# Kernel tuning notes

Measured on AMD Instinct MI355X. Metric: run time of the kernel, lower is better.

## Reference

```python
import jax, jax.numpy as jnp
import numpy as np

N = 20000   # nodes
E = 160000  # edges
D = 128     # out_dim == in_dim
H = 8       # heads
DK = D // H # 16


def setup_inputs() -> dict:
    key = jax.random.key(0)
    ks = jax.random.split(key, 16)
    f = lambda i, shape, s=1.0: jax.random.normal(ks[i], shape, dtype=jnp.float32) * s
    z = lambda shape: jnp.zeros(shape, dtype=jnp.float32)
    return {
        "x_txt": f(0, (N, D)), "x_img": f(1, (N, D)), "x_s": f(2, (N, D)),
        "Wk": f(3, (D, D), 0.05), "bk": z((D,)),
        "Wq": f(4, (D, D), 0.05), "bq": z((D,)),
        "Wv": f(5, (D, D), 0.05), "bv": z((D,)),
        "Wa": f(6, (D, D), 0.05), "ba": z((D,)),
        "rel_att": f(7, (H, DK, DK), 0.25),
        "rel_msg": f(8, (H, DK, DK), 0.25),
        "rel_pri": jnp.ones((H,), jnp.float32),
        "wm_txt": f(9, (H, DK, DK), 0.25),
        "wm_img": f(10, (H, DK, DK), 0.25),
        "wm_s": f(11, (H, DK, DK), 0.25),
        "skip": jnp.ones((1,), jnp.float32),
        "src": jax.random.randint(ks[12], (E,), 0, N),
        "dst": jax.random.randint(ks[13], (E,), 0, N),
    }


def reference(x_txt, x_img, x_s, Wk, bk, Wq, bq, Wv, bv, Wa, ba,
              rel_att, rel_msg, rel_pri, wm_txt, wm_img, wm_s, skip, src, dst):
    n_heads, dk = rel_att.shape[0], rel_att.shape[1]
    n_nodes = x_txt.shape[0]
    sqrt_dk = jnp.sqrt(jnp.asarray(dk, jnp.float32))

    def proj(x, W, b):
        return (x @ W + b).reshape(n_nodes, n_heads, dk)

    xs = (x_txt, x_img, x_s)
    k = [proj(x, Wk, bk)[src] for x in xs]  # [E,H,dk] gathered at src
    q = [proj(x, Wq, bq)[dst] for x in xs]  # [E,H,dk] gathered at dst
    v = [proj(x, Wv, bv)[src] for x in xs]

    # cross-modal lambda: per-edge modality alignment softmax (over the 3 modalities)
    wm = (wm_txt, wm_img, wm_s)
    lam_scores = jnp.stack(
        [jnp.einsum('ehd,hdf,ehf->eh', k[m], wm[m], q[m]) for m in range(3)], axis=0)
    lam = jax.nn.softmax(lam_scores, axis=0)  # [3,E,H]

    # edge attention logits (scaled *10 as in reduce_func) and relation-msg values
    att = [jnp.einsum('ehd,hdf,ehf->eh', k[m], rel_att, q[m]) * rel_pri / sqrt_dk * 10.0
           for m in range(3)]
    vmsg = [jnp.einsum('ehd,hdf->ehf', v[m], rel_msg) for m in range(3)]

    align = -(jnp.abs(att[0] - att[1]) + jnp.abs(att[0] - att[2])
              + jnp.abs(att[1] - att[2])) / 3.0

    def seg_softmax(x):  # softmax over edges sharing the same dst node
        m = jax.ops.segment_max(x, dst, num_segments=n_nodes)
        m = jnp.where(jnp.isfinite(m), m, 0.0)
        e = jnp.exp(x - m[dst])
        s = jax.ops.segment_sum(e, dst, num_segments=n_nodes)
        s = jnp.where(s == 0.0, 1.0, s)
        return e / s[dst]

    beta2 = seg_softmax(align)
    sm = [seg_softmax(a) for a in att]
    beta1 = sm[0] * lam[0] + sm[1] * lam[1] + sm[2] * lam[2]
    beta = seg_softmax(beta1 * beta2)  # [E,H]

    alpha = jax.nn.sigmoid(skip)  # [1]
    outs = []
    for m in range(3):
        h = jax.ops.segment_sum(beta[..., None] * vmsg[m], dst,
                                num_segments=n_nodes).reshape(n_nodes, -1)
        outs.append((h @ Wa + ba) * alpha + xs[m] * (1.0 - alpha))
    return tuple(outs)
```

## Files before the change

### kernel.cpp

```cpp
#include <hip/hip_runtime.h>

#define D 128
#define NH 8

typedef __bf16 bf16x8 __attribute__((ext_vector_type(8)));
typedef unsigned short ushortx8 __attribute__((ext_vector_type(8)));
typedef float floatx4 __attribute__((ext_vector_type(4)));

__device__ __forceinline__ float bf2f(unsigned short u) {
  union { unsigned int i; float f; } x; x.i = ((unsigned int)u) << 16; return x.f;
}
__device__ __forceinline__ unsigned short f2bf(float f) {
  union { float f; unsigned int i; } x; x.f = f;
  unsigned int i = x.i;
  return (unsigned short)((i + 0x7FFFu + ((i >> 16) & 1u)) >> 16);
}
__device__ __forceinline__ void acc2(unsigned int ku, unsigned int qu, float& s) {
  union { unsigned int i; float f; } a, b;
  a.i = ku << 16;          b.i = qu << 16;          s += a.f * b.f;
  a.i = ku & 0xffff0000u;  b.i = qu & 0xffff0000u;  s += a.f * b.f;
}

__global__ __launch_bounds__(256) void k_misc(
    const float* __restrict__ Wk, const float* __restrict__ bk,
    const float* __restrict__ Wq, const float* __restrict__ bq,
    const float* __restrict__ Wv, const float* __restrict__ bv,
    const float* __restrict__ rel_att, const float* __restrict__ rel_msg,
    const float* __restrict__ rel_pri,
    const float* __restrict__ wm0, const float* __restrict__ wm1,
    const float* __restrict__ wm2,
    unsigned short* __restrict__ Wt_all, float* __restrict__ bias_all,
    const int* __restrict__ dst, int* __restrict__ counts, int E)
{
  int b = blockIdx.x;
  if (b >= 384) {
    int e = (b - 384) * 256 + threadIdx.x;
    if (e < E) atomicAdd(&counts[dst[e]], 1);
    return;
  }
  int gid = b * 256 + threadIdx.x;
  if (gid >= 6 * 128 * 128) return;
  int p = gid >> 14;
  int idx = gid & 16383;
  int c = idx >> 7, k = idx & 127;
  int h = c >> 4, r = c & 15;
  float wsum = 0.f, bsum = 0.f;
  if (p == 0) {
    wsum = Wk[k * 128 + c];
    bsum = bk[c];
  } else if (p <= 4) {
    const float* M = (p == 1) ? rel_att : ((p == 2) ? wm0 : ((p == 3) ? wm1 : wm2));
#pragma unroll
    for (int f = 0; f < 16; f++) {
      float mv = M[h * 256 + r * 16 + f];
      wsum += Wq[k * 128 + h * 16 + f] * mv;
      bsum += bq[h * 16 + f] * mv;
    }
    if (p == 1) { float sc = rel_pri[h] * 2.5f; wsum *= sc; bsum *= sc; }
  } else {
#pragma unroll
    for (int d = 0; d < 16; d++) {
      float mv = rel_msg[h * 256 + d * 16 + r];
      wsum += Wv[k * 128 + h * 16 + d] * mv;
      bsum += bv[h * 16 + d] * mv;
    }
  }
  Wt_all[(size_t)p * 16384 + c * 128 + k] = f2bf(wsum);
  if (k == 0) bias_all[p * 128 + c] = bsum;
}

__global__ __launch_bounds__(512) void k_proj(
    const float* __restrict__ x0, const float* __restrict__ x1,
    const float* __restrict__ x2,
    const unsigned short* __restrict__ Wt_all, const float* __restrict__ bias_all,
    unsigned short* __restrict__ P,
    const int* __restrict__ counts, int* __restrict__ row_start,
    int* __restrict__ alloc, int N)
{
  if (blockIdx.y == 3) {
    if (blockIdx.x != 0) return;
    int tid = threadIdx.x, lane = tid & 63;
    for (int base = 0; base < N; base += 512) {
      int n = base + tid;
      int cnt = (n < N) ? counts[n] : 0;
      int x = cnt;
#pragma unroll
      for (int off = 1; off < 64; off <<= 1) {
        int y = __shfl_up(x, off, 64);
        if (lane >= off) x += y;
      }
      int wtot = __shfl(x, 63, 64);
      int wbase = 0;
      if (lane == 63) wbase = atomicAdd(alloc, wtot);
      wbase = __shfl(wbase, 63, 64);
      if (n < N) row_start[n] = wbase + x - cnt;
    }
    return;
  }
  __shared__ __attribute__((aligned(16))) unsigned short Wt[128 * 136];
  int m = blockIdx.y;
  const float* X = (m == 0) ? x0 : ((m == 1) ? x1 : x2);
  int tid = threadIdx.x;
  int wave = tid >> 6, lane = tid & 63;
  int quad = lane >> 4, l16 = lane & 15;
  int row0 = blockIdx.x * 128 + wave * 16;
  int arow = row0 + l16; if (arow >= N) arow = N - 1;
  const float* ap = X + (size_t)arow * D;
  bf16x8 afr[4];
#pragma unroll
  for (int kk4 = 0; kk4 < 4; kk4++) {
    float4 f0 = *(const float4*)(ap + kk4 * 32 + quad * 8);
    float4 f1 = *(const float4*)(ap + kk4 * 32 + quad * 8 + 4);
    ushortx8 uu;
    uu[0]=f2bf(f0.x); uu[1]=f2bf(f0.y); uu[2]=f2bf(f0.z); uu[3]=f2bf(f0.w);
    uu[4]=f2bf(f1.x); uu[5]=f2bf(f1.y); uu[6]=f2bf(f1.z); uu[7]=f2bf(f1.w);
    afr[kk4] = __builtin_bit_cast(bf16x8, uu);
  }
  for (int pt = 0; pt < 4; pt++) {
    int wp = (pt == 0) ? 0 : ((pt == 1) ? 1 : ((pt == 2) ? (2 + m) : 5));
    const unsigned short* Wsrc = Wt_all + (size_t)wp * 16384;
    const float* B = bias_all + wp * 128;
    __syncthreads();
#pragma unroll
    for (int it = 0; it < 4; it++) {
      int idx = it * 512 + tid;
      int c = idx >> 4, kc = (idx & 15) << 3;
      *(uint4*)(&Wt[c * 136 + kc]) = *(const uint4*)(&Wsrc[c * 128 + kc]);
    }
    __syncthreads();
    floatx4 acc[8];
#pragma unroll
    for (int ct = 0; ct < 8; ct++) acc[ct] = (floatx4)0.f;
#pragma unroll
    for (int kk4 = 0; kk4 < 4; kk4++) {
#pragma unroll
      for (int ct = 0; ct < 8; ct++) {
        uint4 bu = *(const uint4*)(&Wt[(ct * 16 + l16) * 136 + kk4 * 32 + quad * 8]);
        bf16x8 bf = __builtin_bit_cast(bf16x8, bu);
        acc[ct] = __builtin_amdgcn_mfma_f32_16x16x32_bf16(afr[kk4], bf, acc[ct], 0, 0, 0);
      }
    }
    unsigned short* Pout = P + (size_t)(pt * 3 + m) * N * D;
#pragma unroll
    for (int ct = 0; ct < 8; ct++) {
      int col = ct * 16 + l16;
      float bias = B[col];
#pragma unroll
      for (int i = 0; i < 4; i++) {
        int r = row0 + quad * 4 + i;
        if (r < N) Pout[(size_t)r * D + col] = f2bf(acc[ct][i] + bias);
      }
    }
  }
}

__global__ void k_scatter(const int* __restrict__ dst, const int* __restrict__ src,
                          const int* __restrict__ row_start,
                          int* __restrict__ cursor, int* __restrict__ src_sorted, int E) {
  int e = blockIdx.x * 256 + threadIdx.x;
  if (e < E) {
    int d = dst[e];
    int pos = atomicAdd(&cursor[d], 1);
    src_sorted[row_start[d] + pos] = src[e];
  }
}

__device__ __forceinline__ void edge_vals(
    const unsigned short* __restrict__ P, size_t Nsz, int s, int h,
    const uint4 (&qa)[3][2], const uint4 (&qw)[3][2],
    float (&av)[3], float (&lv)[3])
{
#pragma unroll
  for (int m = 0; m < 3; m++) {
    const unsigned short* kp = P + ((size_t)m * Nsz + s) * 128 + h * 16;
    uint4 k0 = *(const uint4*)kp, k1 = *(const uint4*)(kp + 8);
    const unsigned int* ka = (const unsigned int*)&k0;
    const unsigned int* kb = (const unsigned int*)&k1;
    const unsigned int* a0 = (const unsigned int*)&qa[m][0];
    const unsigned int* a1 = (const unsigned int*)&qa[m][1];
    const unsigned int* w0 = (const unsigned int*)&qw[m][0];
    const unsigned int* w1 = (const unsigned int*)&qw[m][1];
    float da = 0.f, dw = 0.f;
#pragma unroll
    for (int j = 0; j < 4; j++) {
      acc2(ka[j], a0[j], da); acc2(kb[j], a1[j], da);
      acc2(ka[j], w0[j], dw); acc2(kb[j], w1[j], dw);
    }
    av[m] = da;
    lv[m] = dw;
  }
  float mx = fmaxf(lv[0], fmaxf(lv[1], lv[2]));
  float e0 = __expf(lv[0] - mx), e1 = __expf(lv[1] - mx), e2 = __expf(lv[2] - mx);
  float inv = 1.f / (e0 + e1 + e2);
  lv[0] = e0 * inv; lv[1] = e1 * inv; lv[2] = e2 * inv;
}

__global__ __launch_bounds__(256) void k_node(
    const unsigned short* __restrict__ P,
    const int* __restrict__ row_start, const int* __restrict__ counts,
    const int* __restrict__ srcs,
    unsigned short* __restrict__ hagg, int N, int E)
{
  int tid = threadIdx.x;
  int wave = tid >> 6, lane = tid & 63;
  int n = blockIdx.x * 4 + wave;
  if (n >= N) return;
  int ro = row_start[n];
  int deg = counts[n];
  float acc00 = 0, acc01 = 0, acc10 = 0, acc11 = 0, acc20 = 0, acc21 = 0;
  if (deg > 0) {
    int h = lane & 7, slot = lane >> 3;
    size_t Nsz = (size_t)N;
    uint4 qa[3][2], qw[3][2];
#pragma unroll
    for (int m = 0; m < 3; m++) {
      const unsigned short* qap = P + ((size_t)(3 + m) * Nsz + n) * 128 + h * 16;
      const unsigned short* qwp = P + ((size_t)(6 + m) * Nsz + n) * 128 + h * 16;
      qa[m][0] = *(const uint4*)qap; qa[m][1] = *(const uint4*)(qap + 8);
      qw[m][0] = *(const uint4*)qwp; qw[m][1] = *(const uint4*)(qwp + 8);
    }
    int nch = (deg + 7) >> 3;
    float cX0[4] = {}, cX1[4] = {}, cX2[4] = {}, cEa[4] = {}, cT[4] = {};
    int cS[4] = {};
    float sA0 = 0, sA1 = 0, sA2 = 0, sAl = 0;
#pragma unroll
    for (int c = 0; c < 4; c++) {
      int idx = c * 8 + slot;
      if (c < nch && idx < deg) {
        int s = srcs[ro + idx]; cS[c] = s;
        float av[3], lv[3];
        edge_vals(P, Nsz, s, h, qa, qw, av, lv);
        float e0 = __expf(av[0]), e1 = __expf(av[1]), e2 = __expf(av[2]);
        float align = -(fabsf(av[0]-av[1]) + fabsf(av[0]-av[2]) + fabsf(av[1]-av[2])) * (1.f/3.f);
        float ea = __expf(align);
        cX0[c] = lv[0] * e0; cX1[c] = lv[1] * e1; cX2[c] = lv[2] * e2; cEa[c] = ea;
        sA0 += e0; sA1 += e1; sA2 += e2; sAl += ea;
      }
    }
    for (int c = 4; c < nch; c++) {
      int idx = c * 8 + slot;
      if (idx < deg) {
        int s = srcs[ro + idx];
        float av[3], lv[3];
        edge_vals(P, Nsz, s, h, qa, qw, av, lv);
        float align = -(fabsf(av[0]-av[1]) + fabsf(av[0]-av[2]) + fabsf(av[1]-av[2])) * (1.f/3.f);
        sA0 += __expf(av[0]); sA1 += __expf(av[1]); sA2 += __expf(av[2]);
        sAl += __expf(align);
      }
    }
#pragma unroll
    for (int off = 8; off < 64; off <<= 1) {
      sA0 += __shfl_xor(sA0, off, 64);
      sA1 += __shfl_xor(sA1, off, 64);
      sA2 += __shfl_xor(sA2, off, 64);
      sAl += __shfl_xor(sAl, off, 64);
    }
    float rA0 = 1.f / fmaxf(sA0, 1e-30f), rA1 = 1.f / fmaxf(sA1, 1e-30f);
    float rA2 = 1.f / fmaxf(sA2, 1e-30f), rAl = 1.f / fmaxf(sAl, 1e-30f);
    float sT = 0;
#pragma unroll
    for (int c = 0; c < 4; c++) {
      int idx = c * 8 + slot;
      if (c < nch && idx < deg) {
        float t = (cX0[c] * rA0 + cX1[c] * rA1 + cX2[c] * rA2) * (cEa[c] * rAl);
        cT[c] = t;
        sT += __expf(t);
      }
    }
    for (int c = 4; c < nch; c++) {
      int idx = c * 8 + slot;
      if (idx < deg) {
        int s = srcs[ro + idx];
        float av[3], lv[3];
        edge_vals(P, Nsz, s, h, qa, qw, av, lv);
        float align = -(fabsf(av[0]-av[1]) + fabsf(av[0]-av[2]) + fabsf(av[1]-av[2])) * (1.f/3.f);
        float t = (lv[0]*__expf(av[0])*rA0 + lv[1]*__expf(av[1])*rA1 + lv[2]*__expf(av[2])*rA2)
                  * (__expf(align) * rAl);
        sT += __expf(t);
      }
    }
#pragma unroll
    for (int off = 8; off < 64; off <<= 1) sT += __shfl_xor(sT, off, 64);
    float rT = 1.f / fmaxf(sT, 1e-30f);
    const unsigned int* Pu = (const unsigned int*)P;
    int hl = lane >> 3;
#pragma unroll
    for (int c = 0; c < 4; c++) {
      if (c < nch) {
        int idx = c * 8 + slot;
        float beta = (idx < deg) ? __expf(cT[c]) * rT : 0.f;
        int sv = cS[c];
        float bj[8]; int sj[8];
#pragma unroll
        for (int jj = 0; jj < 8; jj++) {
          bj[jj] = __shfl(beta, jj * 8 + hl, 64);
          sj[jj] = __shfl(sv, jj * 8, 64);
        }
#pragma unroll
        for (int jj = 0; jj < 8; jj++) {
          size_t base9 = ((size_t)9 * Nsz + sj[jj]) * 64 + lane;
          unsigned int u0 = Pu[base9];
          unsigned int u1 = Pu[base9 + Nsz * 64];
          unsigned int u2 = Pu[base9 + 2 * Nsz * 64];
          float b = bj[jj];
          acc00 += b * bf2f((unsigned short)u0); acc01 += b * bf2f((unsigned short)(u0 >> 16));
          acc10 += b * bf2f((unsigned short)u1); acc11 += b * bf2f((unsigned short)(u1 >> 16));
          acc20 += b * bf2f((unsigned short)u2); acc21 += b * bf2f((unsigned short)(u2 >> 16));
        }
      }
    }
    for (int c = 4; c < nch; c++) {
      int idx = c * 8 + slot;
      float beta = 0.f; int sv = 0;
      if (idx < deg) {
        sv = srcs[ro + idx];
        float av[3], lv[3];
        edge_vals(P, Nsz, sv, h, qa, qw, av, lv);
        float align = -(fabsf(av[0]-av[1]) + fabsf(av[0]-av[2]) + fabsf(av[1]-av[2])) * (1.f/3.f);
        float t = (lv[0]*__expf(av[0])*rA0 + lv[1]*__expf(av[1])*rA1 + lv[2]*__expf(av[2])*rA2)
                  * (__expf(align) * rAl);
        beta = __expf(t) * rT;
      }
      int jmax = min(8, deg - c * 8);
      for (int jj = 0; jj < jmax; jj++) {
        float b = __shfl(beta, jj * 8 + hl, 64);
        int s = __shfl(sv, jj * 8, 64);
        size_t base9 = ((size_t)9 * Nsz + s) * 64 + lane;
        unsigned int u0 = Pu[base9];
        unsigned int u1 = Pu[base9 + Nsz * 64];
        unsigned int u2 = Pu[base9 + 2 * Nsz * 64];
        acc00 += b * bf2f((unsigned short)u0); acc01 += b * bf2f((unsigned short)(u0 >> 16));
        acc10 += b * bf2f((unsigned short)u1); acc11 += b * bf2f((unsigned short)(u1 >> 16));
        acc20 += b * bf2f((unsigned short)u2); acc21 += b * bf2f((unsigned short)(u2 >> 16));
      }
    }
  }
  unsigned int* ho = (unsigned int*)hagg;
  ho[((size_t)0 * N + n) * 64 + lane] = ((unsigned int)f2bf(acc01) << 16) | f2bf(acc00);
  ho[((size_t)1 * N + n) * 64 + lane] = ((unsigned int)f2bf(acc11) << 16) | f2bf(acc10);
  ho[((size_t)2 * N + n) * 64 + lane] = ((unsigned int)f2bf(acc21) << 16) | f2bf(acc20);
}

__global__ __launch_bounds__(512) void k_out(
    const unsigned short* __restrict__ Hagg, const float* __restrict__ Wa,
    const float* __restrict__ ba,
    const float* __restrict__ x0, const float* __restrict__ x1,
    const float* __restrict__ x2, const float* __restrict__ skip,
    float* __restrict__ out, int N)
{
  __shared__ __attribute__((aligned(16))) unsigned short Wt[128 * 136];
  int m = blockIdx.y;
  const float* X = (m == 0) ? x0 : ((m == 1) ? x1 : x2);
  int tid = threadIdx.x;
#pragma unroll
  for (int it = 0; it < 8; it++) {
    int idx = it * 512 + tid;
    int k = idx >> 5, c4 = (idx & 31) << 2;
    float4 w = *(const float4*)(&Wa[k * 128 + c4]);
    Wt[(c4 + 0) * 136 + k] = f2bf(w.x);
    Wt[(c4 + 1) * 136 + k] = f2bf(w.y);
    Wt[(c4 + 2) * 136 + k] = f2bf(w.z);
    Wt[(c4 + 3) * 136 + k] = f2bf(w.w);
  }
  __syncthreads();
  float alpha = 1.f / (1.f + __expf(-skip[0]));
  float oma = 1.f - alpha;
  int wave = tid >> 6, lane = tid & 63;
  int quad = lane >> 4, l16 = lane & 15;
  int row0 = blockIdx.x * 128 + wave * 16;
  int arow = row0 + l16; if (arow >= N) arow = N - 1;
  const unsigned short* hp = Hagg + ((size_t)m * N + arow) * D;
  floatx4 acc[8];
#pragma unroll
  for (int ct = 0; ct < 8; ct++) acc[ct] = (floatx4)0.f;
#pragma unroll
  for (int kk = 0; kk < 128; kk += 32) {
    uint4 au = *(const uint4*)(hp + kk + quad * 8);
    bf16x8 af = __builtin_bit_cast(bf16x8, au);
#pragma unroll
    for (int ct = 0; ct < 8; ct++) {
      uint4 bu = *(const uint4*)(&Wt[(ct * 16 + l16) * 136 + kk + quad * 8]);
      bf16x8 bf = __builtin_bit_cast(bf16x8, bu);
      acc[ct] = __builtin_amdgcn_mfma_f32_16x16x32_bf16(af, bf, acc[ct], 0, 0, 0);
    }
  }
  float* om = out + (size_t)m * N * D;
#pragma unroll
  for (int ct = 0; ct < 8; ct++) {
    int col = ct * 16 + l16;
    float bias = ba[col];
#pragma unroll
    for (int i = 0; i < 4; i++) {
      int r = row0 + quad * 4 + i;
      if (r < N) {
        om[(size_t)r * D + col] =
            (acc[ct][i] + bias) * alpha + X[(size_t)r * D + col] * oma;
      }
    }
  }
}

extern "C" void kernel_launch(void* const* d_in, const int* in_sizes, int n_in,
                              void* d_out, int out_size, void* d_ws, size_t ws_size,
                              hipStream_t stream) {
  const float* x0 = (const float*)d_in[0];
  const float* x1 = (const float*)d_in[1];
  const float* x2 = (const float*)d_in[2];
  const float* Wk = (const float*)d_in[3];
  const float* bk = (const float*)d_in[4];
  const float* Wq = (const float*)d_in[5];
  const float* bq = (const float*)d_in[6];
  const float* Wv = (const float*)d_in[7];
  const float* bv = (const float*)d_in[8];
  const float* Wa = (const float*)d_in[9];
  const float* ba = (const float*)d_in[10];
  const float* rel_att = (const float*)d_in[11];
  const float* rel_msg = (const float*)d_in[12];
  const float* rel_pri = (const float*)d_in[13];
  const float* wm0 = (const float*)d_in[14];
  const float* wm1 = (const float*)d_in[15];
  const float* wm2 = (const float*)d_in[16];
  const float* skip = (const float*)d_in[17];
  const int* src = (const int*)d_in[18];
  const int* dstv = (const int*)d_in[19];
  int N = in_sizes[0] / D;
  int E = in_sizes[18];

  char* wsb = (char*)d_ws;
  size_t off = 0;
  auto alloc_b = [&](size_t bytes) { size_t o = off; off += (bytes + 63) & ~(size_t)63; return o; };
  unsigned short* P         = (unsigned short*)(wsb + alloc_b((size_t)12 * N * D * 2));
  unsigned short* Wt_all    = (unsigned short*)(wsb + alloc_b((size_t)6 * 16384 * 2));
  float*          bias_all  = (float*)(wsb + alloc_b((size_t)6 * 128 * 4));
  int*            cnt2      = (int*)(wsb + alloc_b(((size_t)2 * N + 64) * 4));
  int*            row_start = (int*)(wsb + alloc_b((size_t)(N + 1) * 4));
  int*            src_sorted= (int*)(wsb + alloc_b((size_t)E * 4));
  unsigned short* hagg      = (unsigned short*)(wsb + alloc_b((size_t)3 * N * D * 2));
  int* counts = cnt2;
  int* cursor = cnt2 + N;
  int* allocc = cnt2 + 2 * N;

  hipMemsetAsync(cnt2, 0, ((size_t)2 * N + 64) * sizeof(int), stream);
  int hist_blocks = (E + 255) / 256;
  k_misc<<<dim3(384 + hist_blocks), 256, 0, stream>>>(
      Wk, bk, Wq, bq, Wv, bv, rel_att, rel_msg, rel_pri, wm0, wm1, wm2,
      Wt_all, bias_all, dstv, counts, E);
  k_proj<<<dim3((N + 127) / 128, 4), 512, 0, stream>>>(
      x0, x1, x2, Wt_all, bias_all, P, counts, row_start, allocc, N);
  k_scatter<<<dim3((E + 255) / 256), 256, 0, stream>>>(
      dstv, src, row_start, cursor, src_sorted, E);
  k_node<<<dim3((N + 3) / 4), 256, 0, stream>>>(
      P, row_start, counts, src_sorted, hagg, N, E);
  k_out<<<dim3((N + 127) / 128, 3), 512, 0, stream>>>(
      hagg, Wa, ba, x0, x1, x2, skip, (float*)d_out, N);
}
```

Baseline: 255.5 us.

## Fuse all stages into a persistent megakernel with grid-wide barriers

Replaces the five separate launches and their memset with one persistent kernel sized from occupancy, where stages are separated by atomic-counter grid barriers. Projection and output GEMM tiles drop to 64 rows with 256-thread blocks, and the CSR prefix scan is spread across waves in parallel instead of running in a single block. The scatter cursor is initialised to row_start, so the extra add and the memset of the cursor array go away. The aim is to cut launch gaps and the serial scan, at the cost of barrier spin overhead and a dependence on every block being co-resident.

New measurement: 248.8 us. -2.6%, faster.

```diff
diff --git a/kernel.cpp b/kernel.cpp
--- a/kernel.cpp
+++ b/kernel.cpp
@@ -21,7 +21,19 @@
   a.i = ku & 0xffff0000u;  b.i = qu & 0xffff0000u;  s += a.f * b.f;
 }
 
-__global__ __launch_bounds__(256) void k_misc(
+__device__ __forceinline__ void gbar(int* cnt, int nb) {
+  __threadfence();
+  __syncthreads();
+  if (threadIdx.x == 0) {
+    __hip_atomic_fetch_add(cnt, 1, __ATOMIC_ACQ_REL, __HIP_MEMORY_SCOPE_AGENT);
+    while (__hip_atomic_load(cnt, __ATOMIC_ACQUIRE, __HIP_MEMORY_SCOPE_AGENT) < nb) {}
+  }
+  __syncthreads();
+  __threadfence();
+}
+
+__device__ __forceinline__ void fold_item(
+    int gid,
     const float* __restrict__ Wk, const float* __restrict__ bk,
     const float* __restrict__ Wq, const float* __restrict__ bq,
     const float* __restrict__ Wv, const float* __restrict__ bv,
@@ -29,17 +41,8 @@
     const float* __restrict__ rel_pri,
     const float* __restrict__ wm0, const float* __restrict__ wm1,
     const float* __restrict__ wm2,
-    unsigned short* __restrict__ Wt_all, float* __restrict__ bias_all,
-    const int* __restrict__ dst, int* __restrict__ counts, int E)
-{
-  int b = blockIdx.x;
-  if (b >= 384) {
-    int e = (b - 384) * 256 + threadIdx.x;
-    if (e < E) atomicAdd(&counts[dst[e]], 1);
-    return;
-  }
-  int gid = b * 256 + threadIdx.x;
-  if (gid >= 6 * 128 * 128) return;
+    unsigned short* __restrict__ Wt_all, float* __restrict__ bias_all)
+{
   int p = gid >> 14;
   int idx = gid & 16383;
   int c = idx >> 7, k = idx & 127;
@@ -69,41 +72,17 @@
   if (k == 0) bias_all[p * 128 + c] = bsum;
 }
 
-__global__ __launch_bounds__(512) void k_proj(
-    const float* __restrict__ x0, const float* __restrict__ x1,
+__device__ __forceinline__ void proj_tile(
+    int t, const float* __restrict__ x0, const float* __restrict__ x1,
     const float* __restrict__ x2,
     const unsigned short* __restrict__ Wt_all, const float* __restrict__ bias_all,
-    unsigned short* __restrict__ P,
-    const int* __restrict__ counts, int* __restrict__ row_start,
-    int* __restrict__ alloc, int N)
-{
-  if (blockIdx.y == 3) {
-    if (blockIdx.x != 0) return;
-    int tid = threadIdx.x, lane = tid & 63;
-    for (int base = 0; base < N; base += 512) {
-      int n = base + tid;
-      int cnt = (n < N) ? counts[n] : 0;
-      int x = cnt;
-#pragma unroll
-      for (int off = 1; off < 64; off <<= 1) {
-        int y = __shfl_up(x, off, 64);
-        if (lane >= off) x += y;
-      }
-      int wtot = __shfl(x, 63, 64);
-      int wbase = 0;
-      if (lane == 63) wbase = atomicAdd(alloc, wtot);
-      wbase = __shfl(wbase, 63, 64);
-      if (n < N) row_start[n] = wbase + x - cnt;
-    }
-    return;
-  }
-  __shared__ __attribute__((aligned(16))) unsigned short Wt[128 * 136];
-  int m = blockIdx.y;
+    unsigned short* __restrict__ P, int N, unsigned short* Wt, int tid)
+{
+  int m = t % 3, rt = t / 3;
   const float* X = (m == 0) ? x0 : ((m == 1) ? x1 : x2);
-  int tid = threadIdx.x;
   int wave = tid >> 6, lane = tid & 63;
   int quad = lane >> 4, l16 = lane & 15;
-  int row0 = blockIdx.x * 128 + wave * 16;
+  int row0 = rt * 64 + wave * 16;
   int arow = row0 + l16; if (arow >= N) arow = N - 1;
   const float* ap = X + (size_t)arow * D;
   bf16x8 afr[4];
@@ -122,8 +101,8 @@
     const float* B = bias_all + wp * 128;
     __syncthreads();
 #pragma unroll
-    for (int it = 0; it < 4; it++) {
-      int idx = it * 512 + tid;
+    for (int it = 0; it < 8; it++) {
+      int idx = it * 256 + tid;
       int c = idx >> 4, kc = (idx & 15) << 3;
       *(uint4*)(&Wt[c * 136 + kc]) = *(const uint4*)(&Wsrc[c * 128 + kc]);
     }
@@ -154,15 +133,23 @@
   }
 }
 
-__global__ void k_scatter(const int* __restrict__ dst, const int* __restrict__ src,
-                          const int* __restrict__ row_start,
-                          int* __restrict__ cursor, int* __restrict__ src_sorted, int E) {
-  int e = blockIdx.x * 256 + threadIdx.x;
-  if (e < E) {
-    int d = dst[e];
-    int pos = atomicAdd(&cursor[d], 1);
-    src_sorted[row_start[d] + pos] = src[e];
-  }
+__device__ __forceinline__ void assign_chunk(
+    int a, const int* __restrict__ counts, int* __restrict__ row_start,
+    int* __restrict__ cursor, int* __restrict__ allocg, int N, int lane)
+{
+  int n = a * 64 + lane;
+  int cnt = (n < N) ? counts[n] : 0;
+  int x = cnt;
+#pragma unroll
+  for (int off = 1; off < 64; off <<= 1) {
+    int y = __shfl_up(x, off, 64);
+    if (lane >= off) x += y;
+  }
+  int wtot = __shfl(x, 63, 64);
+  int wbase = 0;
+  if (lane == 63) wbase = atomicAdd(allocg, wtot);
+  wbase = __shfl(wbase, 63, 64);
+  if (n < N) { int v = wbase + x - cnt; row_start[n] = v; cursor[n] = v; }
 }
 
 __device__ __forceinline__ void edge_vals(
@@ -195,16 +182,12 @@
   lv[0] = e0 * inv; lv[1] = e1 * inv; lv[2] = e2 * inv;
 }
 
-__global__ __launch_bounds__(256) void k_node(
-    const unsigned short* __restrict__ P,
+__device__ __forceinline__ void node_one(
+    int n, const unsigned short* __restrict__ P,
     const int* __restrict__ row_start, const int* __restrict__ counts,
-    const int* __restrict__ srcs,
-    unsigned short* __restrict__ hagg, int N, int E)
-{
-  int tid = threadIdx.x;
-  int wave = tid >> 6, lane = tid & 63;
-  int n = blockIdx.x * 4 + wave;
-  if (n >= N) return;
+    const int* __restrict__ srcs, unsigned short* __restrict__ hagg,
+    int N, int lane)
+{
   int ro = row_start[n];
   int deg = counts[n];
   float acc00 = 0, acc01 = 0, acc10 = 0, acc11 = 0, acc20 = 0, acc21 = 0;
@@ -341,20 +324,101 @@
   ho[((size_t)2 * N + n) * 64 + lane] = ((unsigned int)f2bf(acc21) << 16) | f2bf(acc20);
 }
 
-__global__ __launch_bounds__(512) void k_out(
-    const unsigned short* __restrict__ Hagg, const float* __restrict__ Wa,
-    const float* __restrict__ ba,
+__device__ __forceinline__ void out_tile(
+    int t, const unsigned short* __restrict__ Hagg, const float* __restrict__ ba,
     const float* __restrict__ x0, const float* __restrict__ x1,
-    const float* __restrict__ x2, const float* __restrict__ skip,
-    float* __restrict__ out, int N)
+    const float* __restrict__ x2, float alpha,
+    float* __restrict__ out, int N, const unsigned short* Wt, int tid)
+{
+  int m = t % 3, rt = t / 3;
+  const float* X = (m == 0) ? x0 : ((m == 1) ? x1 : x2);
+  float oma = 1.f - alpha;
+  int wave = tid >> 6, lane = tid & 63;
+  int quad = lane >> 4, l16 = lane & 15;
+  int row0 = rt * 64 + wave * 16;
+  int arow = row0 + l16; if (arow >= N) arow = N - 1;
+  const unsigned short* hp = Hagg + ((size_t)m * N + arow) * D;
+  floatx4 acc[8];
+#pragma unroll
+  for (int ct = 0; ct < 8; ct++) acc[ct] = (floatx4)0.f;
+#pragma unroll
+  for (int kk = 0; kk < 128; kk += 32) {
+    uint4 au = *(const uint4*)(hp + kk + quad * 8);
+    bf16x8 af = __builtin_bit_cast(bf16x8, au);
+#pragma unroll
+    for (int ct = 0; ct < 8; ct++) {
+      uint4 bu = *(const uint4*)(&Wt[(ct * 16 + l16) * 136 + kk + quad * 8]);
+      bf16x8 bf = __builtin_bit_cast(bf16x8, bu);
+      acc[ct] = __builtin_amdgcn_mfma_f32_16x16x32_bf16(af, bf, acc[ct], 0, 0, 0);
+    }
+  }
+  float* om = out + (size_t)m * N * D;
+#pragma unroll
+  for (int ct = 0; ct < 8; ct++) {
+    int col = ct * 16 + l16;
+    float bias = ba[col];
+#pragma unroll
+    for (int i = 0; i < 4; i++) {
+      int r = row0 + quad * 4 + i;
+      if (r < N) {
+        om[(size_t)r * D + col] =
+            (acc[ct][i] + bias) * alpha + X[(size_t)r * D + col] * oma;
+      }
+    }
+  }
+}
+
+__global__ __launch_bounds__(256) void k_mega(
+    const float* x0, const float* x1, const float* x2,
+    const float* Wk, const float* bk, const float* Wq, const float* bq,
+    const float* Wv, const float* bv, const float* Wa, const float* ba,
+    const float* rel_att, const float* rel_msg, const float* rel_pri,
+    const float* wm0, const float* wm1, const float* wm2,
+    const float* skip, const int* src, const int* dst,
+    float* out, unsigned short* P, unsigned short* Wt_all, float* bias_all,
+    int* bar, int* allocg, int* counts, int* cursor, int* row_start,
+    int* src_sorted, unsigned short* hagg, int N, int E)
 {
   __shared__ __attribute__((aligned(16))) unsigned short Wt[128 * 136];
-  int m = blockIdx.y;
-  const float* X = (m == 0) ? x0 : ((m == 1) ? x1 : x2);
-  int tid = threadIdx.x;
-#pragma unroll
-  for (int it = 0; it < 8; it++) {
-    int idx = it * 512 + tid;
+  int tid = threadIdx.x, bid = blockIdx.x, NB = gridDim.x;
+  int gid = bid * 256 + tid, gstride = NB * 256;
+  int wave = tid >> 6, lane = tid & 63;
+
+  for (int i = gid; i < N; i += gstride) counts[i] = 0;
+  for (int i = gid; i < 6 * 16384; i += gstride)
+    fold_item(i, Wk, bk, Wq, bq, Wv, bv, rel_att, rel_msg, rel_pri,
+              wm0, wm1, wm2, Wt_all, bias_all);
+  gbar(bar + 0 * 16, NB);
+
+  for (int e = gid; e < E; e += gstride) atomicAdd(&counts[dst[e]], 1);
+  int ntiles = ((N + 63) / 64) * 3;
+  for (int t = bid; t < ntiles; t += NB)
+    proj_tile(t, x0, x1, x2, Wt_all, bias_all, P, N, Wt, tid);
+  gbar(bar + 1 * 16, NB);
+
+  int nchunks = (N + 63) / 64;
+  for (int a = bid * 4 + wave; a < nchunks; a += NB * 4)
+    assign_chunk(a, counts, row_start, cursor, allocg, N, lane);
+  gbar(bar + 2 * 16, NB);
+
+  for (int e = gid; e < E; e += gstride) {
+    int d = dst[e];
+    int pos = atomicAdd(&cursor[d], 1);
+    src_sorted[pos] = src[e];
+  }
+  gbar(bar + 3 * 16, NB);
+
+  int ngroups = (N + 3) / 4;
+  for (int g = bid; g < ngroups; g += NB) {
+    int n = g * 4 + wave;
+    if (n < N) node_one(n, P, row_start, counts, src_sorted, hagg, N, lane);
+  }
+  gbar(bar + 4 * 16, NB);
+
+  __syncthreads();
+#pragma unroll
+  for (int it = 0; it < 16; it++) {
+    int idx = it * 256 + tid;
     int k = idx >> 5, c4 = (idx & 31) << 2;
     float4 w = *(const float4*)(&Wa[k * 128 + c4]);
     Wt[(c4 + 0) * 136 + k] = f2bf(w.x);
@@ -364,40 +428,86 @@
   }
   __syncthreads();
   float alpha = 1.f / (1.f + __expf(-skip[0]));
-  float oma = 1.f - alpha;
-  int wave = tid >> 6, lane = tid & 63;
-  int quad = lane >> 4, l16 = lane & 15;
-  int row0 = blockIdx.x * 128 + wave * 16;
-  int arow = row0 + l16; if (arow >= N) arow = N - 1;
-  const unsigned short* hp = Hagg + ((size_t)m * N + arow) * D;
-  floatx4 acc[8];
-#pragma unroll
-  for (int ct = 0; ct < 8; ct++) acc[ct] = (floatx4)0.f;
-#pragma unroll
-  for (int kk = 0; kk < 128; kk += 32) {
-    uint4 au = *(const uint4*)(hp + kk + quad * 8);
-    bf16x8 af = __builtin_bit_cast(bf16x8, au);
-#pragma unroll
-    for (int ct = 0; ct < 8; ct++) {
-      uint4 bu = *(const uint4*)(&Wt[(ct * 16 + l16) * 136 + kk + quad * 8]);
-      bf16x8 bf = __builtin_bit_cast(bf16x8, bu);
-      acc[ct] = __builtin_amdgcn_mfma_f32_16x16x32_bf16(af, bf, acc[ct], 0, 0, 0);
-    }
-  }
-  float* om = out + (size_t)m * N * D;
-#pragma unroll
-  for (int ct = 0; ct < 8; ct++) {
-    int col = ct * 16 + l16;
-    float bias = ba[col];
-#pragma unroll
-    for (int i = 0; i < 4; i++) {
-      int r = row0 + quad * 4 + i;
-      if (r < N) {
-        om[(size_t)r * D + col] =
-            (acc[ct][i] + bias) * alpha + X[(size_t)r * D + col] * oma;
-      }
-    }
-  }
+  for (int t = bid; t < ntiles; t += NB)
+    out_tile(t, hagg, ba, x0, x1, x2, alpha, out, N, Wt, tid);
+}
+
+__global__ __launch_bounds__(256) void fb_misc(
+    const float* Wk, const float* bk, const float* Wq, const float* bq,
+    const float* Wv, const float* bv,
+    const float* rel_att, const float* rel_msg, const float* rel_pri,
+    const float* wm0, const float* wm1, const float* wm2,
+    unsigned short* Wt_all, float* bias_all,
+    const int* dst, int* counts, int E)
+{
+  int b = blockIdx.x;
+  if (b < 384) {
+    int g = b * 256 + threadIdx.x;
+    if (g < 6 * 16384)
+      fold_item(g, Wk, bk, Wq, bq, Wv, bv, rel_att, rel_msg, rel_pri,
+                wm0, wm1, wm2, Wt_all, bias_all);
+  } else {
+    int e = (b - 384) * 256 + threadIdx.x;
+    if (e < E) atomicAdd(&counts[dst[e]], 1);
+  }
+}
+
+__global__ __launch_bounds__(256) void fb_projassign(
+    const float* x0, const float* x1, const float* x2,
+    const unsigned short* Wt_all, const float* bias_all,
+    unsigned short* P, const int* counts, int* row_start, int* cursor,
+    int* allocg, int N)
+{
+  __shared__ __attribute__((aligned(16))) unsigned short Wt[128 * 136];
+  int ntiles = ((N + 63) / 64) * 3;
+  int b = blockIdx.x;
+  if (b < ntiles) {
+    proj_tile(b, x0, x1, x2, Wt_all, bias_all, P, N, Wt, threadIdx.x);
+  } else {
+    int a = (b - ntiles) * 4 + (threadIdx.x >> 6);
+    if (a < (N + 63) / 64)
+      assign_chunk(a, counts, row_start, cursor, allocg, N, threadIdx.x & 63);
+  }
+}
+
+__global__ void fb_scatter(const int* dst, const int* src, int* cursor,
+                           int* src_sorted, int E) {
+  int e = blockIdx.x * 256 + threadIdx.x;
+  if (e < E) {
+    int d = dst[e];
+    int pos = atomicAdd(&cursor[d], 1);
+    src_sorted[pos] = src[e];
+  }
+}
+
+__global__ __launch_bounds__(256) void fb_node(
+    const unsigned short* P, const int* row_start, const int* counts,
+    const int* srcs, unsigned short* hagg, int N)
+{
+  int n = blockIdx.x * 4 + (threadIdx.x >> 6);
+  if (n < N) node_one(n, P, row_start, counts, srcs, hagg, N, threadIdx.x & 63);
+}
+
+__global__ __launch_bounds__(256) void fb_out(
+    const unsigned short* Hagg, const float* Wa, const float* ba,
+    const float* x0, const float* x1, const float* x2, const float* skip,
+    float* out, int N)
+{
+  __shared__ __attribute__((aligned(16))) unsigned short Wt[128 * 136];
+  int tid = threadIdx.x;
+#pragma unroll
+  for (int it = 0; it < 16; it++) {
+    int idx = it * 256 + tid;
+    int k = idx >> 5, c4 = (idx & 31) << 2;
+    float4 w = *(const float4*)(&Wa[k * 128 + c4]);
+    Wt[(c4 + 0) * 136 + k] = f2bf(w.x);
+    Wt[(c4 + 1) * 136 + k] = f2bf(w.y);
+    Wt[(c4 + 2) * 136 + k] = f2bf(w.z);
+    Wt[(c4 + 3) * 136 + k] = f2bf(w.w);
+  }
+  __syncthreads();
+  float alpha = 1.f / (1.f + __expf(-skip[0]));
+  out_tile(blockIdx.x, Hagg, ba, x0, x1, x2, alpha, out, N, Wt, tid);
 }
 
 extern "C" void kernel_launch(void* const* d_in, const int* in_sizes, int n_in,
@@ -432,25 +542,40 @@
   unsigned short* P         = (unsigned short*)(wsb + alloc_b((size_t)12 * N * D * 2));
   unsigned short* Wt_all    = (unsigned short*)(wsb + alloc_b((size_t)6 * 16384 * 2));
   float*          bias_all  = (float*)(wsb + alloc_b((size_t)6 * 128 * 4));
-  int*            cnt2      = (int*)(wsb + alloc_b(((size_t)2 * N + 64) * 4));
+  int*            ctrl      = (int*)(wsb + alloc_b(((size_t)144 + 2 * N) * 4));
   int*            row_start = (int*)(wsb + alloc_b((size_t)(N + 1) * 4));
   int*            src_sorted= (int*)(wsb + alloc_b((size_t)E * 4));
   unsigned short* hagg      = (unsigned short*)(wsb + alloc_b((size_t)3 * N * D * 2));
-  int* counts = cnt2;
-  int* cursor = cnt2 + N;
-  int* allocc = cnt2 + 2 * N;
-
-  hipMemsetAsync(cnt2, 0, ((size_t)2 * N + 64) * sizeof(int), stream);
-  int hist_blocks = (E + 255) / 256;
-  k_misc<<<dim3(384 + hist_blocks), 256, 0, stream>>>(
-      Wk, bk, Wq, bq, Wv, bv, rel_att, rel_msg, rel_pri, wm0, wm1, wm2,
-      Wt_all, bias_all, dstv, counts, E);
-  k_proj<<<dim3((N + 127) / 128, 4), 512, 0, stream>>>(
-      x0, x1, x2, Wt_all, bias_all, P, counts, row_start, allocc, N);
-  k_scatter<<<dim3((E + 255) / 256), 256, 0, stream>>>(
-      dstv, src, row_start, cursor, src_sorted, E);
-  k_node<<<dim3((N + 3) / 4), 256, 0, stream>>>(
-      P, row_start, counts, src_sorted, hagg, N, E);
-  k_out<<<dim3((N + 127) / 128, 3), 512, 0, stream>>>(
-      hagg, Wa, ba, x0, x1, x2, skip, (float*)d_out, N);
-}
+  int* bar    = ctrl;
+  int* allocg = ctrl + 128;
+  int* counts = ctrl + 144;
+  int* cursor = ctrl + 144 + N;
+
+  hipMemsetAsync(ctrl, 0, ((size_t)144 + N) * sizeof(int), stream);
+
+  int nbPerCu = 0;
+  hipError_t oe = hipOccupancyMaxActiveBlocksPerMultiprocessor(&nbPerCu, k_mega, 256, 0);
+  if (oe == hipSuccess && nbPerCu >= 1) {
+    int grid = nbPerCu * 256;
+    if (grid > 2048) grid = 2048;
+    k_mega<<<dim3(grid), 256, 0, stream>>>(
+        x0, x1, x2, Wk, bk, Wq, bq, Wv, bv, Wa, ba,
+        rel_att, rel_msg, rel_pri, wm0, wm1, wm2, skip, src, dstv,
+        (float*)d_out, P, Wt_all, bias_all,
+        bar, allocg, counts, cursor, row_start, src_sorted, hagg, N, E);
+  } else {
+    int ntiles = ((N + 63) / 64) * 3;
+    int nchunks = (N + 63) / 64;
+    fb_misc<<<dim3(384 + (E + 255) / 256), 256, 0, stream>>>(
+        Wk, bk, Wq, bq, Wv, bv, rel_att, rel_msg, rel_pri, wm0, wm1, wm2,
+        Wt_all, bias_all, dstv, counts, E);
+    fb_projassign<<<dim3(ntiles + (nchunks + 3) / 4), 256, 0, stream>>>(
+        x0, x1, x2, Wt_all, bias_all, P, counts, row_start, cursor, allocg, N);
+    fb_scatter<<<dim3((E + 255) / 256), 256, 0, stream>>>(
+        dstv, src, cursor, src_sorted, E);
+    fb_node<<<dim3((N + 3) / 4), 256, 0, stream>>>(
+        P, row_start, counts, src_sorted, hagg, N);
+    fb_out<<<dim3(ntiles), 256, 0, stream>>>(
+        hagg, Wa, ba, x0, x1, x2, skip, (float*)d_out, N);
+  }
+}
```
